# Kernel optimization log

Hardware: AMD Instinct MI355X
Metric: run time of the kernel (lower is better)

Reference implementation:

```python
import jax, jax.numpy as jnp
import numpy as np

N = 8192      # atoms
E = 4096      # edges (become transformer tokens)
E2 = 65536    # edges of second graph y
VOCAB = 119
DE = 200      # node_features == embedding_dim
D = 256
H = 8
L = 2
DFF = 2048


def _bn(x, g, b, eps=1e-6):
    m = x.mean(0)
    v = x.var(0)
    return (x - m) * jax.lax.rsqrt(v + eps) * g + b


def _ln(x, g, b, eps=1e-5):
    m = x.mean(-1, keepdims=True)
    v = ((x - m) ** 2).mean(-1, keepdims=True)
    return (x - m) * jax.lax.rsqrt(v + eps) * g + b


def _gcn(x, ei, W, b):
    # PyG GCNConv: add self loops, symmetric deg^-1/2 normalization
    n = x.shape[0]
    loop = jnp.arange(n)
    src = jnp.concatenate([ei[0], loop])
    dst = jnp.concatenate([ei[1], loop])
    deg = jax.ops.segment_sum(jnp.ones(src.shape[0], x.dtype), dst, num_segments=n)
    dinv = jnp.where(deg > 0, jax.lax.rsqrt(jnp.maximum(deg, 1e-12)), 0.0)
    msg = (x @ W)[src] * (dinv[src] * dinv[dst])[:, None]
    return jax.ops.segment_sum(msg, dst, num_segments=n) + b


def _mha(x, wi, bi, wo, bo):
    S, d = x.shape
    dh = d // H
    q, k, v = jnp.split(x @ wi + bi, 3, axis=1)
    q = q.reshape(S, H, dh)
    k = k.reshape(S, H, dh)
    v = v.reshape(S, H, dh)
    sc = jnp.einsum('qhd,khd->hqk', q, k) * (1.0 / np.sqrt(dh))
    a = jax.nn.softmax(sc, axis=-1)
    o = jnp.einsum('hqk,khd->qhd', a, v).reshape(S, d)
    return o @ wo + bo


def setup_inputs() -> dict:
    key = jax.random.key(0)
    ks = iter(jax.random.split(key, 64))
    nrm = lambda shape, s=0.05: jax.random.normal(next(ks), shape, jnp.float32) * s
    d = {}
    d['x'] = jax.random.randint(next(ks), (N,), 0, VOCAB)
    d['edge_index'] = jax.random.randint(next(ks), (2, E), 1, N + 1)  # 1-based, code subtracts 1
    d['pos'] = jax.random.normal(next(ks), (N, 3), jnp.float32)
    d['y'] = jax.random.randint(next(ks), (2, E2), 0, E)
    d['emb'] = nrm((VOCAB, DE), 1.0)
    d['fc1_w'] = nrm((1, DE))
    d['fc1_b'] = jnp.zeros((DE,), jnp.float32)
    d['bn4_g'] = jnp.ones((DE,), jnp.float32)
    d['bn4_b'] = jnp.zeros((DE,), jnp.float32)
    d['conv1_w'] = nrm((DE, D))
    d['conv1_b'] = jnp.zeros((D,), jnp.float32)
    d['conv2_w'] = nrm((D, D))
    d['conv2_b'] = jnp.zeros((D,), jnp.float32)
    for i in (1, 2, 3):
        d['bn%d_g' % i] = jnp.ones((D,), jnp.float32)
        d['bn%d_b' % i] = jnp.zeros((D,), jnp.float32)
    d['in_proj_w'] = nrm((L, D, 3 * D))
    d['in_proj_b'] = jnp.zeros((L, 3 * D), jnp.float32)
    d['out_proj_w'] = nrm((L, D, D))
    d['out_proj_b'] = jnp.zeros((L, D), jnp.float32)
    d['ln1_g'] = jnp.ones((L, D), jnp.float32)
    d['ln1_b'] = jnp.zeros((L, D), jnp.float32)
    d['ln2_g'] = jnp.ones((L, D), jnp.float32)
    d['ln2_b'] = jnp.zeros((L, D), jnp.float32)
    d['ff1_w'] = nrm((L, D, DFF))
    d['ff1_b'] = jnp.zeros((L, DFF), jnp.float32)
    d['ff2_w'] = nrm((L, DFF, D))
    d['ff2_b'] = jnp.zeros((L, D), jnp.float32)
    d['fc3_w'] = nrm((D, 1))
    d['fc3_b'] = jnp.zeros((1,), jnp.float32)
    d['fc4_w'] = nrm((D, 9))
    d['fc4_b'] = jnp.zeros((9,), jnp.float32)
    return d


def reference(x, edge_index, pos, y, emb, fc1_w, fc1_b, bn4_g, bn4_b,
              conv1_w, conv1_b, conv2_w, conv2_b,
              bn1_g, bn1_b, bn2_g, bn2_b, bn3_g, bn3_b,
              in_proj_w, in_proj_b, out_proj_w, out_proj_b,
              ln1_g, ln1_b, ln2_g, ln2_b, ff1_w, ff1_b, ff2_w, ff2_b,
              fc3_w, fc3_b, fc4_w, fc4_b):
    h = emb[x]                                   # [N, DE]
    ei = edge_index - 1
    row, col = ei[0], ei[1]
    ef = jnp.linalg.norm(pos[col] - pos[row], axis=1, keepdims=True)  # [E,1]
    ef = _bn(ef @ fc1_w + fc1_b, bn4_g, bn4_b)   # [E, DE]
    h = h[row] + h[col] + ef                     # [E, DE] edges -> tokens
    h = jax.nn.leaky_relu(_gcn(h, y, conv1_w, conv1_b))
    h = _bn(h, bn1_g, bn1_b)
    h = jax.nn.leaky_relu(h + _gcn(h, y, conv2_w, conv2_b))
    h = _bn(h, bn2_g, bn2_b)
    # post-norm TransformerEncoder (unbatched seq of length E), dropout=0
    for i in range(L):
        h = _ln(h + _mha(h, in_proj_w[i], in_proj_b[i], out_proj_w[i], out_proj_b[i]),
                ln1_g[i], ln1_b[i])
        ff = jax.nn.relu(h @ ff1_w[i] + ff1_b[i]) @ ff2_w[i] + ff2_b[i]
        h = _ln(h + ff, ln2_g[i], ln2_b[i])
    h = jax.nn.leaky_relu(h)
    h = _bn(h, bn3_g, bn3_b)
    sym_out = h @ fc3_w + fc3_b
    asym_out = h @ fc4_w + fc4_b
    return (sym_out, asym_out)
```

## Files before the change

### kernel.cpp

```cpp
#include <hip/hip_runtime.h>
#include <math.h>

#define ETOK 4096
#define NE2  65536
#define DEF  200
#define DM   256
#define NH   8
#define DH   32
#define DFFN 2048
#define NKS  8

#define QSCALE_LOG2E 0.25503474f

typedef __attribute__((ext_vector_type(8))) short bfrag8;
typedef __attribute__((ext_vector_type(4))) float f32x4;
typedef __attribute__((ext_vector_type(4))) short short4v;
typedef __attribute__((ext_vector_type(4))) unsigned int u32x4;

__device__ __forceinline__ unsigned short f2bf(float f) {
  union { float f; unsigned u; } v; v.f = f;
  unsigned u = v.u + 0x7fffu + ((v.u >> 16) & 1u);
  return (unsigned short)(u >> 16);
}
__device__ __forceinline__ float bf2f(unsigned short u) {
  union { unsigned u; float f; } v;
  v.u = ((unsigned)u) << 16;
  return v.f;
}
__device__ __forceinline__ unsigned cvt_pk_bf16(float lo, float hi) {
  unsigned r;
  asm("v_cvt_pk_bf16_f32 %0, %1, %2" : "=v"(r) : "v"(lo), "v"(hi));
  return r;
}

__device__ __forceinline__ float wave_sum(float v) {
#pragma unroll
  for (int off = 32; off > 0; off >>= 1) v += __shfl_xor(v, off);
  return v;
}
__device__ __forceinline__ float block_sum(float v, float* red) {
  v = wave_sum(v);
  int lane = threadIdx.x & 63, w = threadIdx.x >> 6;
  if (lane == 0) red[w] = v;
  __syncthreads();
  float t = red[0] + red[1] + red[2] + red[3];
  __syncthreads();
  return t;
}

__global__ void edge_deg_kernel(const int* __restrict__ ei, const float* __restrict__ pos,
                                float* __restrict__ ef0, float* __restrict__ stats,
                                const int* __restrict__ y, int* __restrict__ deg) {
  __shared__ float red[4];
  int e2 = blockIdx.x * 256 + threadIdx.x;
  atomicAdd(&deg[y[NE2 + e2]], 1);
  if (blockIdx.x < 16) {
    int e = blockIdx.x * 256 + threadIdx.x;
    int r = ei[e] - 1;
    int c = ei[ETOK + e] - 1;
    float dx = pos[c * 3 + 0] - pos[r * 3 + 0];
    float dy = pos[c * 3 + 1] - pos[r * 3 + 1];
    float dz = pos[c * 3 + 2] - pos[r * 3 + 2];
    float d = sqrtf(dx * dx + dy * dy + dz * dz);
    ef0[e] = d;
    float s = block_sum(d, red);
    float s2 = block_sum(d * d, red);
    if (threadIdx.x == 0) {
      atomicAdd(stats + 0, s);
      atomicAdd(stats + 1, s2);
    }
  }
}

__global__ void token_build_kernel(const int* __restrict__ x, const int* __restrict__ ei,
                                   const float* __restrict__ emb, const float* __restrict__ fc1_w,
                                   const float* __restrict__ bn4_g, const float* __restrict__ bn4_b,
                                   const float* __restrict__ ef0, const float* __restrict__ stats,
                                   unsigned short* __restrict__ tokbf) {
  int e = blockIdx.x;
  int j = threadIdx.x;
  float m = stats[0] * (1.0f / 4096.0f);
  float v = stats[1] * (1.0f / 4096.0f) - m * m;
  int xr = x[ei[e] - 1];
  int xc = x[ei[ETOK + e] - 1];
  float dd = ef0[e] - m;
  float val = 0.f;
  if (j < DEF) {
    float w = fc1_w[j];
    float s = w * rsqrtf(v * w * w + 1e-6f) * bn4_g[j];
    val = emb[(size_t)xr * DEF + j] + emb[(size_t)xc * DEF + j] + dd * s + bn4_b[j];
  }
  tokbf[(size_t)e * 256 + j] = f2bf(val);
}

__global__ void scan_kernel(const int* __restrict__ deg, int* __restrict__ off,
                            int* __restrict__ cursor, float* __restrict__ dinv) {
  __shared__ int part[256];
  int t = threadIdx.x;
  int v[16];
  int s = 0;
#pragma unroll
  for (int i = 0; i < 16; ++i) {
    v[i] = deg[t * 16 + i];
    s += v[i];
  }
  part[t] = s;
  __syncthreads();
  if (t == 0) {
    int a = 0;
#pragma unroll 1
    for (int i = 0; i < 256; ++i) {
      int tmp = part[i];
      part[i] = a;
      a += tmp;
    }
    off[4096] = a;
  }
  __syncthreads();
  int a = part[t];
#pragma unroll
  for (int i = 0; i < 16; ++i) {
    off[t * 16 + i] = a;
    cursor[t * 16 + i] = a;
    dinv[t * 16 + i] = rsqrtf((float)(v[i] + 1));
    a += v[i];
  }
}
__global__ void fill_kernel(const int* __restrict__ y, int* __restrict__ cursor,
                            int* __restrict__ srcl) {
  int e = blockIdx.x * 256 + threadIdx.x;
  int s = y[e];
  int d = y[NE2 + e];
  int slot = atomicAdd(&cursor[d], 1);
  srcl[slot] = s;
}

template <int RES, int ACT>
__global__ __launch_bounds__(256) void gather_kernel(const float* __restrict__ xw,
                                                     const int* __restrict__ off,
                                                     const int* __restrict__ srcl,
                                                     const float* __restrict__ dinv,
                                                     const float* __restrict__ bias,
                                                     const float* __restrict__ resid,
                                                     float* __restrict__ out) {
  __shared__ int slds[256];
  __shared__ float dlds[256];
  const int d = blockIdx.x;
  const int c = threadIdx.x;
  const int b0 = off[d], b1 = off[d + 1];
  const float dd = dinv[d];
  float acc = 0.f;
  for (int base = b0; base < b1; base += 256) {
    int n = min(256, b1 - base);
    __syncthreads();
    if (c < n) {
      int s = srcl[base + c];
      slds[c] = s;
      dlds[c] = dinv[s];
    }
    __syncthreads();
    for (int j = 0; j < n; ++j) {
      int s = slds[j];
      acc = fmaf(xw[(size_t)s * DM + c], dlds[j], acc);
    }
  }
  size_t idx = (size_t)d * DM + c;
  float v = bias[c] + xw[idx] * dd * dd + acc * dd;
  if (RES) v += resid[idx];
  if (ACT) v = v > 0.f ? v : 0.01f * v;
  out[idx] = v;
}

struct WEntry {
  const float* src;
  unsigned short* dst;
  int K, N, KP, tilesN, ntiles;
};
struct WPack {
  WEntry e[10];
};
__global__ __launch_bounds__(256) void wtrans_all_kernel(WPack p) {
  __shared__ float tl[32][33];
  int t = blockIdx.x;
  int i = 0;
  while (t >= p.e[i].ntiles) {
    t -= p.e[i].ntiles;
    ++i;
  }
  const WEntry w = p.e[i];
  int nb = (t % w.tilesN) * 32;
  int kb = (t / w.tilesN) * 32;
  int tx = threadIdx.x & 31, ty = threadIdx.x >> 5;
#pragma unroll
  for (int r = ty; r < 32; r += 8) {
    int k = kb + r, n = nb + tx;
    tl[r][tx] = (k < w.K && n < w.N) ? w.src[(size_t)k * w.N + n] : 0.f;
  }
  __syncthreads();
#pragma unroll
  for (int r = ty; r < 32; r += 8) {
    int n = nb + r, k = kb + tx;
    if (n < w.N) w.dst[(size_t)n * w.KP + k] = f2bf(tl[tx][r]);
  }
}

template <int BM, int BN, int OUTBF, int ACT, int QS, int VSPLIT>
__global__ __launch_bounds__(256) void mfma_gemm(const unsigned short* __restrict__ A,
                                                 const unsigned short* __restrict__ Bt,
                                                 const float* __restrict__ bias,
                                                 void* __restrict__ Cout, void* __restrict__ Cout2,
                                                 int M, int N, int K) {
  constexpr int BK = 64;
  constexpr int TM = BM / 32, TN = BN / 32;
  constexpr int ACH = BM / 32, BCH = BN / 32;
  __shared__ unsigned short Alds[BM * BK];
  __shared__ unsigned short Blds[BN * BK];
  const int tid = threadIdx.x;
  const int lane = tid & 63, wid = tid >> 6;
  const int g = lane >> 4, q = lane & 15;
  const int wr = wid >> 1, wc = wid & 1;
  const int m0 = blockIdx.y * BM, n0 = blockIdx.x * BN;

  f32x4 acc[TM][TN];
#pragma unroll
  for (int i = 0; i < TM; ++i)
#pragma unroll
    for (int j = 0; j < TN; ++j) acc[i][j] = (f32x4){0.f, 0.f, 0.f, 0.f};

  for (int k0 = 0; k0 < K; k0 += BK) {
    __syncthreads();
#pragma unroll
    for (int c = 0; c < ACH; ++c) {
      int chunk = wid * ACH + c;
      int row = chunk * 8 + (lane >> 3);
      int cb = ((lane & 7) * 16) ^ ((row & 7) << 4);
      const char* gp = (const char*)A + ((size_t)(m0 + row) * K + k0) * 2 + cb;
      __builtin_amdgcn_global_load_lds(
          (const __attribute__((address_space(1))) unsigned int*)gp,
          (__attribute__((address_space(3))) unsigned int*)(Alds + chunk * 512), 16, 0, 0);
    }
#pragma unroll
    for (int c = 0; c < BCH; ++c) {
      int chunk = wid * BCH + c;
      int row = chunk * 8 + (lane >> 3);
      int cb = ((lane & 7) * 16) ^ ((row & 7) << 4);
      const char* gp = (const char*)Bt + ((size_t)(n0 + row) * K + k0) * 2 + cb;
      __builtin_amdgcn_global_load_lds(
          (const __attribute__((address_space(1))) unsigned int*)gp,
          (__attribute__((address_space(3))) unsigned int*)(Blds + chunk * 512), 16, 0, 0);
    }
    __syncthreads();
#pragma unroll
    for (int ks = 0; ks < 2; ++ks) {
      bfrag8 af[TM], bfr[TN];
#pragma unroll
      for (int mi = 0; mi < TM; ++mi) {
        int row = wr * (BM / 2) + mi * 16 + q;
        int cb = (ks * 64 + g * 16) ^ ((row & 7) << 4);
        af[mi] = *(const bfrag8*)((const char*)Alds + row * 128 + cb);
      }
#pragma unroll
      for (int ni = 0; ni < TN; ++ni) {
        int row = wc * (BN / 2) + ni * 16 + q;
        int cb = (ks * 64 + g * 16) ^ ((row & 7) << 4);
        bfr[ni] = *(const bfrag8*)((const char*)Blds + row * 128 + cb);
      }
#pragma unroll
      for (int mi = 0; mi < TM; ++mi)
#pragma unroll
        for (int ni = 0; ni < TN; ++ni)
          acc[mi][ni] = __builtin_amdgcn_mfma_f32_16x16x32_bf16(af[mi], bfr[ni], acc[mi][ni], 0, 0, 0);
    }
  }
#pragma unroll
  for (int mi = 0; mi < TM; ++mi) {
    int row = m0 + wr * (BM / 2) + mi * 16 + g * 4;
#pragma unroll
    for (int ni = 0; ni < TN; ++ni) {
      int col = n0 + wc * (BN / 2) + ni * 16 + q;
      float bv = bias ? bias[col] : 0.f;
      if (VSPLIT && col >= 512) {
        short4v pkv;
#pragma unroll
        for (int r = 0; r < 4; ++r) pkv[r] = (short)f2bf(acc[mi][ni][r] + bv);
        *(short4v*)((unsigned short*)Cout2 + (size_t)(col - 512) * M + row) = pkv;
      } else {
#pragma unroll
        for (int r = 0; r < 4; ++r) {
          float v = acc[mi][ni][r] + bv;
          if (QS && col < DM) v *= QSCALE_LOG2E;
          if (ACT == 1) v = fmaxf(v, 0.f);
          if (OUTBF)
            ((unsigned short*)Cout)[(size_t)(row + r) * (VSPLIT ? 512 : N) + col] = f2bf(v);
          else
            ((float*)Cout)[(size_t)(row + r) * N + col] = v;
        }
      }
    }
  }
}

template <int LEAKY>
__global__ __launch_bounds__(256) void col_accum_kernel(const float* __restrict__ x,
                                                        float* __restrict__ colm,
                                                        float* __restrict__ colv) {
  int c = threadIdx.x;
  int r0 = blockIdx.x * 16;
  float s = 0.f, s2 = 0.f;
#pragma unroll
  for (int i = 0; i < 16; ++i) {
    float v = x[(size_t)(r0 + i) * DM + c];
    if (LEAKY) v = v > 0.f ? v : 0.01f * v;
    s += v;
    s2 += v * v;
  }
  atomicAdd(&colm[c], s);
  atomicAdd(&colv[c], s2);
}
template <int LEAKY>
__global__ void bn_apply_kernel(const float* __restrict__ x, const float* __restrict__ colm,
                                const float* __restrict__ colv, const float* __restrict__ g,
                                const float* __restrict__ b, float* __restrict__ outf,
                                unsigned short* __restrict__ outb, int C) {
  size_t i = (size_t)blockIdx.x * 256 + threadIdx.x;
  int c = (int)(i % C);
  float mean = colm[c] * (1.0f / 4096.0f);
  float var = colv[c] * (1.0f / 4096.0f) - mean * mean;
  float v0 = x[i];
  if (LEAKY) v0 = v0 > 0.f ? v0 : 0.01f * v0;
  float v = (v0 - mean) * rsqrtf(var + 1e-6f) * g[c] + b[c];
  outf[i] = v;
  if (outb) outb[i] = f2bf(v);
}

__global__ __launch_bounds__(256, 6) void attn_mfma_kernel(const unsigned short* __restrict__ qk,
                                                           const unsigned short* __restrict__ vt,
                                                           unsigned short* __restrict__ Opart,
                                                           float* __restrict__ Lpart) {
  const int h = blockIdx.y;
  const int qblk = blockIdx.x * 128;
  const int chunk = blockIdx.z;
  const int tid = threadIdx.x;
  const int wid = tid >> 6, lane = tid & 63;
  const int g = lane >> 4, q = lane & 15;

  __shared__ unsigned short Klds[64][40];
  __shared__ unsigned int Vtw[32][36];
  __shared__ unsigned short Plds[4][32][40];

  bfrag8 qfrag0, qfrag1;
  {
    const unsigned short* qp = qk + (size_t)(qblk + wid * 32 + q) * 512 + h * DH + g * 8;
    qfrag0 = *(const bfrag8*)qp;
    qfrag1 = *(const bfrag8*)(qp + 16 * 512);
  }
  bfrag8 ones;
#pragma unroll
  for (int i = 0; i < 8; ++i) ones[i] = (short)0x3F80;
  const f32x4 zero = {0.f, 0.f, 0.f, 0.f};

  const int skey = tid >> 2;
  const int sdb = (tid & 3) * 8;
  const int sd = tid >> 3;
  const int sk4 = (tid & 7) * 4;

  const int kbeg = chunk * (ETOK / NKS);
  const int NT = (ETOK / NKS) / 64;

  const unsigned short* kptr = qk + (size_t)(kbeg + skey) * 512 + DM + h * DH + sdb;
  const unsigned short* vptr = vt + (size_t)(h * DH + sd) * ETOK + kbeg + sk4 * 2;

  bfrag8 kreg = *(const bfrag8*)kptr;
  kptr += (size_t)64 * 512;
  u32x4 vreg = *(const u32x4*)vptr;
  vptr += 64;

  f32x4 o00 = zero, o01 = zero, o10 = zero, o11 = zero;
  f32x4 ol0 = zero, ol1 = zero;

  for (int t = 0; t < NT; ++t) {
    *(bfrag8*)&Klds[skey][sdb] = kreg;
    *(u32x4*)&Vtw[sd][sk4] = vreg;
    __syncthreads();
    if (t + 1 < NT) {
      kreg = *(const bfrag8*)kptr;
      kptr += (size_t)64 * 512;
      vreg = *(const u32x4*)vptr;
      vptr += 64;
    }

#pragma unroll
    for (int kg = 0; kg < 2; ++kg) {
      f32x4 s0a, s0b, s1a, s1b;
      __builtin_amdgcn_s_setprio(1);
      {
        bfrag8 kfa = *(const bfrag8*)&Klds[(2 * kg) * 16 + q][g * 8];
        bfrag8 kfb = *(const bfrag8*)&Klds[(2 * kg + 1) * 16 + q][g * 8];
        s0a = __builtin_amdgcn_mfma_f32_16x16x32_bf16(kfa, qfrag0, zero, 0, 0, 0);
        s1a = __builtin_amdgcn_mfma_f32_16x16x32_bf16(kfa, qfrag1, zero, 0, 0, 0);
        s0b = __builtin_amdgcn_mfma_f32_16x16x32_bf16(kfb, qfrag0, zero, 0, 0, 0);
        s1b = __builtin_amdgcn_mfma_f32_16x16x32_bf16(kfb, qfrag1, zero, 0, 0, 0);
      }
      __builtin_amdgcn_s_setprio(0);

      {
        uint2 w2;
        w2.x = cvt_pk_bf16(__builtin_exp2f(s0a[0]), __builtin_exp2f(s0a[1]));
        w2.y = cvt_pk_bf16(__builtin_exp2f(s0a[2]), __builtin_exp2f(s0a[3]));
        *(uint2*)&Plds[wid][q][g * 4] = w2;
        w2.x = cvt_pk_bf16(__builtin_exp2f(s0b[0]), __builtin_exp2f(s0b[1]));
        w2.y = cvt_pk_bf16(__builtin_exp2f(s0b[2]), __builtin_exp2f(s0b[3]));
        *(uint2*)&Plds[wid][q][16 + g * 4] = w2;
        w2.x = cvt_pk_bf16(__builtin_exp2f(s1a[0]), __builtin_exp2f(s1a[1]));
        w2.y = cvt_pk_bf16(__builtin_exp2f(s1a[2]), __builtin_exp2f(s1a[3]));
        *(uint2*)&Plds[wid][16 + q][g * 4] = w2;
        w2.x = cvt_pk_bf16(__builtin_exp2f(s1b[0]), __builtin_exp2f(s1b[1]));
        w2.y = cvt_pk_bf16(__builtin_exp2f(s1b[2]), __builtin_exp2f(s1b[3]));
        *(uint2*)&Plds[wid][16 + q][16 + g * 4] = w2;
      }

      __builtin_amdgcn_s_setprio(1);
      {
        bfrag8 pa0 = *(const bfrag8*)&Plds[wid][q][g * 8];
        bfrag8 pa1 = *(const bfrag8*)&Plds[wid][16 + q][g * 8];
        bfrag8 vb0 = *(const bfrag8*)&Vtw[q][kg * 16 + g * 4];
        bfrag8 vb1 = *(const bfrag8*)&Vtw[16 + q][kg * 16 + g * 4];
        o00 = __builtin_amdgcn_mfma_f32_16x16x32_bf16(pa0, vb0, o00, 0, 0, 0);
        o01 = __builtin_amdgcn_mfma_f32_16x16x32_bf16(pa0, vb1, o01, 0, 0, 0);
        o10 = __builtin_amdgcn_mfma_f32_16x16x32_bf16(pa1, vb0, o10, 0, 0, 0);
        o11 = __builtin_amdgcn_mfma_f32_16x16x32_bf16(pa1, vb1, o11, 0, 0, 0);
        ol0 = __builtin_amdgcn_mfma_f32_16x16x32_bf16(pa0, ones, ol0, 0, 0, 0);
        ol1 = __builtin_amdgcn_mfma_f32_16x16x32_bf16(pa1, ones, ol1, 0, 0, 0);
      }
      __builtin_amdgcn_s_setprio(0);
    }
    __syncthreads();
  }

#pragma unroll
  for (int r = 0; r < 4; ++r) {
    int row0 = qblk + wid * 32 + g * 4 + r;
    unsigned short* op0 = Opart + ((size_t)chunk * ETOK + row0) * DM + h * DH;
    op0[q] = f2bf(o00[r]);
    op0[16 + q] = f2bf(o01[r]);
    unsigned short* op1 = op0 + (size_t)16 * DM;
    op1[q] = f2bf(o10[r]);
    op1[16 + q] = f2bf(o11[r]);
  }
  if (q == 0) {
#pragma unroll
    for (int r = 0; r < 4; ++r) {
      int row = qblk + wid * 32 + g * 4 + r;
      Lpart[((size_t)chunk * ETOK + row) * NH + h] = ol0[r];
      Lpart[((size_t)chunk * ETOK + row + 16) * NH + h] = ol1[r];
    }
  }
}

__global__ __launch_bounds__(256) void attn_combine_kernel(const unsigned short* __restrict__ Opart,
                                                           const float* __restrict__ Lpart,
                                                           unsigned short* __restrict__ out) {
  __shared__ float ls[NKS][NH];
  const int row = blockIdx.x;
  const int c = threadIdx.x;
  if (c < NKS * NH) {
    ls[c >> 3][c & 7] = Lpart[((size_t)(c >> 3) * ETOK + row) * NH + (c & 7)];
  }
  __syncthreads();
  const int h = c >> 5;
  float lstar = 0.f, acc = 0.f;
#pragma unroll
  for (int ch = 0; ch < NKS; ++ch) {
    lstar += ls[ch][h];
    acc += bf2f(Opart[((size_t)ch * ETOK + row) * DM + c]);
  }
  out[(size_t)row * DM + c] = f2bf(acc / lstar);
}

__global__ void add_ln_kernel(const float* __restrict__ x, const float* __restrict__ r,
                              float* __restrict__ outf, unsigned short* __restrict__ outb,
                              const float* __restrict__ g, const float* __restrict__ b) {
  __shared__ float red[4];
  int row = blockIdx.x, t = threadIdx.x;
  size_t idx = (size_t)row * DM + t;
  float v = x[idx] + r[idx];
  float mean = block_sum(v, red) * (1.0f / 256.0f);
  float dv = v - mean;
  float var = block_sum(dv * dv, red) * (1.0f / 256.0f);
  float o = dv * rsqrtf(var + 1e-5f) * g[t] + b[t];
  outf[idx] = o;
  outb[idx] = f2bf(o);
}

__global__ void head_kernel(const float* __restrict__ h, const float* __restrict__ colm,
                            const float* __restrict__ colv, const float* __restrict__ bng,
                            const float* __restrict__ bnb, const float* __restrict__ fc3w,
                            const float* __restrict__ fc3b, const float* __restrict__ fc4w,
                            const float* __restrict__ fc4b, float* __restrict__ out) {
  int wave = threadIdx.x >> 6, lane = threadIdx.x & 63;
  int tok = blockIdx.x * 4 + wave;
  const float* hr = h + (size_t)tok * DM;
  float hv[4];
#pragma unroll
  for (int i = 0; i < 4; ++i) {
    int col = lane * 4 + i;
    float v = hr[col];
    v = v > 0.f ? v : 0.01f * v;
    float mean = colm[col] * (1.0f / 4096.0f);
    float var = colv[col] * (1.0f / 4096.0f) - mean * mean;
    hv[i] = (v - mean) * rsqrtf(var + 1e-6f) * bng[col] + bnb[col];
  }
  float acc = 0.f;
#pragma unroll
  for (int i = 0; i < 4; ++i) acc += hv[i] * fc3w[lane * 4 + i];
  acc = wave_sum(acc);
  if (lane == 0) out[tok] = acc + fc3b[0];
#pragma unroll
  for (int j = 0; j < 9; ++j) {
    float a = 0.f;
#pragma unroll
    for (int i = 0; i < 4; ++i) a += hv[i] * fc4w[(lane * 4 + i) * 9 + j];
    a = wave_sum(a);
    if (lane == 0) out[ETOK + (size_t)tok * 9 + j] = a + fc4b[j];
  }
}

extern "C" void kernel_launch(void* const* d_in, const int* in_sizes, int n_in,
                              void* d_out, int out_size, void* d_ws, size_t ws_size,
                              hipStream_t stream) {
  const int* x = (const int*)d_in[0];
  const int* edge_index = (const int*)d_in[1];
  const float* pos = (const float*)d_in[2];
  const int* y = (const int*)d_in[3];
  const float* emb = (const float*)d_in[4];
  const float* fc1_w = (const float*)d_in[5];
  const float* bn4_g = (const float*)d_in[7];
  const float* bn4_b = (const float*)d_in[8];
  const float* conv1_w = (const float*)d_in[9];
  const float* conv1_b = (const float*)d_in[10];
  const float* conv2_w = (const float*)d_in[11];
  const float* conv2_b = (const float*)d_in[12];
  const float* bn1_g = (const float*)d_in[13];
  const float* bn1_b = (const float*)d_in[14];
  const float* bn2_g = (const float*)d_in[15];
  const float* bn2_b = (const float*)d_in[16];
  const float* bn3_g = (const float*)d_in[17];
  const float* bn3_b = (const float*)d_in[18];
  const float* ipw = (const float*)d_in[19];
  const float* ipb = (const float*)d_in[20];
  const float* opw = (const float*)d_in[21];
  const float* opb = (const float*)d_in[22];
  const float* ln1_g = (const float*)d_in[23];
  const float* ln1_b = (const float*)d_in[24];
  const float* ln2_g = (const float*)d_in[25];
  const float* ln2_b = (const float*)d_in[26];
  const float* ff1w = (const float*)d_in[27];
  const float* ff1b = (const float*)d_in[28];
  const float* ff2w = (const float*)d_in[29];
  const float* ff2b = (const float*)d_in[30];
  const float* fc3w = (const float*)d_in[31];
  const float* fc3b = (const float*)d_in[32];
  const float* fc4w = (const float*)d_in[33];
  const float* fc4b = (const float*)d_in[34];
  float* outp = (float*)d_out;

  char* wsp = (char*)d_ws;
  auto alloc = [&](size_t bytes) {
    void* p = (void*)wsp;
    wsp += (bytes + 255) & ~(size_t)255;
    return p;
  };
  unsigned short* big_bf = (unsigned short*)alloc((size_t)ETOK * DFFN * 2);
  unsigned short* qk_bf = (unsigned short*)alloc((size_t)ETOK * 512 * 2);
  unsigned short* vt_bf = (unsigned short*)alloc((size_t)DM * ETOK * 2);
  unsigned short* attno = (unsigned short*)alloc((size_t)ETOK * DM * 2);
  unsigned short* h_bf = (unsigned short*)alloc((size_t)ETOK * DM * 2);
  unsigned short* tok_bf = (unsigned short*)alloc((size_t)ETOK * 256 * 2);
  float* hf = (float*)alloc((size_t)ETOK * DM * 4);
  float* t1 = (float*)alloc((size_t)ETOK * DM * 4);
  float* t2 = (float*)alloc((size_t)ETOK * DM * 4);
  unsigned short* Opart = (unsigned short*)alloc((size_t)NKS * ETOK * DM * 2);
  float* Lpart = (float*)alloc((size_t)NKS * ETOK * NH * 4);
  unsigned short* c1wt = (unsigned short*)alloc(256 * 256 * 2);
  unsigned short* c2wt = (unsigned short*)alloc(256 * 256 * 2);
  unsigned short* ipwt = (unsigned short*)alloc((size_t)2 * 768 * 256 * 2);
  unsigned short* opwt = (unsigned short*)alloc((size_t)2 * 256 * 256 * 2);
  unsigned short* f1wt = (unsigned short*)alloc((size_t)2 * 2048 * 256 * 2);
  unsigned short* f2wt = (unsigned short*)alloc((size_t)2 * 256 * 2048 * 2);
  float* ef0 = (float*)alloc(ETOK * 4);
  float* dinv = (float*)alloc(ETOK * 4);
  int* off = (int*)alloc((ETOK + 1) * 4);
  int* cursor = (int*)alloc(ETOK * 4);
  int* srcl = (int*)alloc(NE2 * 4);
  char* z0 = wsp;
  float* stats = (float*)alloc(8 * 4);
  float* colm = (float*)alloc(3 * DM * 4);
  float* colv = (float*)alloc(3 * DM * 4);
  int* deg = (int*)alloc(ETOK * 4);
  size_t zlen = (char*)wsp - z0;

  hipMemsetAsync(z0, 0, zlen, stream);

  WPack wp;
  int ntot = 0;
  auto went = [&](int i, const float* src, unsigned short* dst, int K, int N, int KP) {
    wp.e[i].src = src;
    wp.e[i].dst = dst;
    wp.e[i].K = K;
    wp.e[i].N = N;
    wp.e[i].KP = KP;
    wp.e[i].tilesN = (N + 31) / 32;
    wp.e[i].ntiles = ((N + 31) / 32) * (KP / 32);
    ntot += wp.e[i].ntiles;
  };
  went(0, conv1_w, c1wt, 200, 256, 256);
  went(1, conv2_w, c2wt, 256, 256, 256);
  went(2, ipw, ipwt, 256, 768, 256);
  went(3, ipw + (size_t)256 * 768, ipwt + (size_t)768 * 256, 256, 768, 256);
  went(4, opw, opwt, 256, 256, 256);
  went(5, opw + (size_t)256 * 256, opwt + (size_t)256 * 256, 256, 256, 256);
  went(6, ff1w, f1wt, 256, 2048, 256);
  went(7, ff1w + (size_t)256 * 2048, f1wt + (size_t)2048 * 256, 256, 2048, 256);
  went(8, ff2w, f2wt, 2048, 256, 2048);
  went(9, ff2w + (size_t)2048 * 256, f2wt + (size_t)256 * 2048, 2048, 256, 2048);
  wtrans_all_kernel<<<ntot, 256, 0, stream>>>(wp);

  edge_deg_kernel<<<NE2 / 256, 256, 0, stream>>>(edge_index, pos, ef0, stats, y, deg);
  scan_kernel<<<1, 256, 0, stream>>>(deg, off, cursor, dinv);
  fill_kernel<<<NE2 / 256, 256, 0, stream>>>(y, cursor, srcl);
  token_build_kernel<<<ETOK, 256, 0, stream>>>(x, edge_index, emb, fc1_w, bn4_g, bn4_b, ef0,
                                               stats, tok_bf);

  mfma_gemm<64, 32, 0, 0, 0, 0><<<dim3(8, 64), 256, 0, stream>>>(tok_bf, c1wt, nullptr, t1,
                                                                 nullptr, ETOK, DM, 256);
  gather_kernel<0, 1><<<ETOK, 256, 0, stream>>>(t1, off, srcl, dinv, conv1_b, nullptr, t2);
  col_accum_kernel<0><<<ETOK / 16, 256, 0, stream>>>(t2, colm, colv);
  bn_apply_kernel<0><<<ETOK * DM / 256, 256, 0, stream>>>(t2, colm, colv, bn1_g, bn1_b, hf, h_bf, DM);

  mfma_gemm<64, 32, 0, 0, 0, 0><<<dim3(8, 64), 256, 0, stream>>>(h_bf, c2wt, nullptr, t1,
                                                                 nullptr, ETOK, DM, 256);
  gather_kernel<1, 1><<<ETOK, 256, 0, stream>>>(t1, off, srcl, dinv, conv2_b, hf, t2);
  col_accum_kernel<0><<<ETOK / 16, 256, 0, stream>>>(t2, colm + DM, colv + DM);
  bn_apply_kernel<0><<<ETOK * DM / 256, 256, 0, stream>>>(t2, colm + DM, colv + DM, bn2_g, bn2_b,
                                                          hf, h_bf, DM);

  for (int i = 0; i < 2; ++i) {
    mfma_gemm<64, 32, 1, 0, 1, 1><<<dim3(24, 64), 256, 0, stream>>>(
        h_bf, ipwt + (size_t)i * 768 * 256, ipb + (size_t)i * 768, qk_bf, vt_bf, ETOK, 768, 256);
    attn_mfma_kernel<<<dim3(ETOK / 128, NH, NKS), 256, 0, stream>>>(qk_bf, vt_bf, Opart, Lpart);
    attn_combine_kernel<<<ETOK, 256, 0, stream>>>(Opart, Lpart, attno);
    mfma_gemm<64, 32, 0, 0, 0, 0><<<dim3(8, 64), 256, 0, stream>>>(
        attno, opwt + (size_t)i * 256 * 256, opb + (size_t)i * DM, t2, nullptr, ETOK, DM, 256);
    add_ln_kernel<<<ETOK, 256, 0, stream>>>(t2, hf, hf, h_bf, ln1_g + (size_t)i * DM,
                                            ln1_b + (size_t)i * DM);
    mfma_gemm<64, 64, 1, 1, 0, 0><<<dim3(32, 64), 256, 0, stream>>>(
        h_bf, f1wt + (size_t)i * 2048 * 256, ff1b + (size_t)i * DFFN, big_bf, nullptr, ETOK, DFFN, 256);
    mfma_gemm<64, 32, 0, 0, 0, 0><<<dim3(8, 64), 256, 0, stream>>>(
        big_bf, f2wt + (size_t)i * 256 * 2048, ff2b + (size_t)i * DM, t2, nullptr, ETOK, DM, 2048);
    add_ln_kernel<<<ETOK, 256, 0, stream>>>(t2, hf, hf, h_bf, ln2_g + (size_t)i * DM,
                                            ln2_b + (size_t)i * DM);
  }

  col_accum_kernel<1><<<ETOK / 16, 256, 0, stream>>>(hf, colm + 2 * DM, colv + 2 * DM);
  head_kernel<<<ETOK / 4, 256, 0, stream>>>(hf, colm + 2 * DM, colv + 2 * DM, bn3_g, bn3_b,
                                            fc3w, fc3b, fc4w, fc4b, outp);
}
```

Measured before the change: 321.4 us.

## Double attention query tile per block to reuse K/V tiles across more queries

```diff
diff --git a/kernel.cpp b/kernel.cpp
--- a/kernel.cpp
+++ b/kernel.cpp
@@ -333,12 +333,12 @@
   if (outb) outb[i] = f2bf(v);
 }
 
-__global__ __launch_bounds__(256, 6) void attn_mfma_kernel(const unsigned short* __restrict__ qk,
+__global__ __launch_bounds__(256, 4) void attn_mfma_kernel(const unsigned short* __restrict__ qk,
                                                            const unsigned short* __restrict__ vt,
                                                            unsigned short* __restrict__ Opart,
                                                            float* __restrict__ Lpart) {
   const int h = blockIdx.y;
-  const int qblk = blockIdx.x * 128;
+  const int qblk = blockIdx.x * 256;
   const int chunk = blockIdx.z;
   const int tid = threadIdx.x;
   const int wid = tid >> 6, lane = tid & 63;
@@ -346,13 +346,14 @@
 
   __shared__ unsigned short Klds[64][40];
   __shared__ unsigned int Vtw[32][36];
-  __shared__ unsigned short Plds[4][32][40];
-
-  bfrag8 qfrag0, qfrag1;
-  {
-    const unsigned short* qp = qk + (size_t)(qblk + wid * 32 + q) * 512 + h * DH + g * 8;
-    qfrag0 = *(const bfrag8*)qp;
-    qfrag1 = *(const bfrag8*)(qp + 16 * 512);
+  __shared__ unsigned short Plds[4][16][40];
+
+  bfrag8 qfrag[4];
+#pragma unroll
+  for (int qf = 0; qf < 4; ++qf) {
+    const unsigned short* qp =
+        qk + (size_t)(qblk + wid * 64 + qf * 16 + q) * 512 + h * DH + g * 8;
+    qfrag[qf] = *(const bfrag8*)qp;
   }
   bfrag8 ones;
 #pragma unroll
@@ -375,8 +376,14 @@
   u32x4 vreg = *(const u32x4*)vptr;
   vptr += 64;
 
-  f32x4 o00 = zero, o01 = zero, o10 = zero, o11 = zero;
-  f32x4 ol0 = zero, ol1 = zero;
+  f32x4 o[4][2];
+  f32x4 ol[4];
+#pragma unroll
+  for (int qf = 0; qf < 4; ++qf) {
+    o[qf][0] = zero;
+    o[qf][1] = zero;
+    ol[qf] = zero;
+  }
 
   for (int t = 0; t < NT; ++t) {
     *(bfrag8*)&Klds[skey][sdb] = kreg;
@@ -390,69 +397,57 @@
     }
 
 #pragma unroll
-    for (int kg = 0; kg < 2; ++kg) {
-      f32x4 s0a, s0b, s1a, s1b;
+    for (int qf = 0; qf < 4; ++qf) {
+      f32x4 s[4];
       __builtin_amdgcn_s_setprio(1);
-      {
-        bfrag8 kfa = *(const bfrag8*)&Klds[(2 * kg) * 16 + q][g * 8];
-        bfrag8 kfb = *(const bfrag8*)&Klds[(2 * kg + 1) * 16 + q][g * 8];
-        s0a = __builtin_amdgcn_mfma_f32_16x16x32_bf16(kfa, qfrag0, zero, 0, 0, 0);
-        s1a = __builtin_amdgcn_mfma_f32_16x16x32_bf16(kfa, qfrag1, zero, 0, 0, 0);
-        s0b = __builtin_amdgcn_mfma_f32_16x16x32_bf16(kfb, qfrag0, zero, 0, 0, 0);
-        s1b = __builtin_amdgcn_mfma_f32_16x16x32_bf16(kfb, qfrag1, zero, 0, 0, 0);
+#pragma unroll
+      for (int tt = 0; tt < 4; ++tt) {
+        bfrag8 kf = *(const bfrag8*)&Klds[tt * 16 + q][g * 8];
+        s[tt] = __builtin_amdgcn_mfma_f32_16x16x32_bf16(kf, qfrag[qf], zero, 0, 0, 0);
       }
       __builtin_amdgcn_s_setprio(0);
 
-      {
-        uint2 w2;
-        w2.x = cvt_pk_bf16(__builtin_exp2f(s0a[0]), __builtin_exp2f(s0a[1]));
-        w2.y = cvt_pk_bf16(__builtin_exp2f(s0a[2]), __builtin_exp2f(s0a[3]));
-        *(uint2*)&Plds[wid][q][g * 4] = w2;
-        w2.x = cvt_pk_bf16(__builtin_exp2f(s0b[0]), __builtin_exp2f(s0b[1]));
-        w2.y = cvt_pk_bf16(__builtin_exp2f(s0b[2]), __builtin_exp2f(s0b[3]));
-        *(uint2*)&Plds[wid][q][16 + g * 4] = w2;
-        w2.x = cvt_pk_bf16(__builtin_exp2f(s1a[0]), __builtin_exp2f(s1a[1]));
-        w2.y = cvt_pk_bf16(__builtin_exp2f(s1a[2]), __builtin_exp2f(s1a[3]));
-        *(uint2*)&Plds[wid][16 + q][g * 4] = w2;
-        w2.x = cvt_pk_bf16(__builtin_exp2f(s1b[0]), __builtin_exp2f(s1b[1]));
-        w2.y = cvt_pk_bf16(__builtin_exp2f(s1b[2]), __builtin_exp2f(s1b[3]));
-        *(uint2*)&Plds[wid][16 + q][16 + g * 4] = w2;
+#pragma unroll
+      for (int kg = 0; kg < 2; ++kg) {
+        {
+          uint2 w2;
+          w2.x = cvt_pk_bf16(__builtin_exp2f(s[2 * kg][0]), __builtin_exp2f(s[2 * kg][1]));
+          w2.y = cvt_pk_bf16(__builtin_exp2f(s[2 * kg][2]), __builtin_exp2f(s[2 * kg][3]));
+          *(uint2*)&Plds[wid][q][g * 4] = w2;
+          w2.x = cvt_pk_bf16(__builtin_exp2f(s[2 * kg + 1][0]), __builtin_exp2f(s[2 * kg + 1][1]));
+          w2.y = cvt_pk_bf16(__builtin_exp2f(s[2 * kg + 1][2]), __builtin_exp2f(s[2 * kg + 1][3]));
+          *(uint2*)&Plds[wid][q][16 + g * 4] = w2;
+        }
+        __builtin_amdgcn_s_setprio(1);
+        {
+          bfrag8 pa = *(const bfrag8*)&Plds[wid][q][g * 8];
+          bfrag8 vb0 = *(const bfrag8*)&Vtw[q][kg * 16 + g * 4];
+          bfrag8 vb1 = *(const bfrag8*)&Vtw[16 + q][kg * 16 + g * 4];
+          o[qf][0] = __builtin_amdgcn_mfma_f32_16x16x32_bf16(pa, vb0, o[qf][0], 0, 0, 0);
+          o[qf][1] = __builtin_amdgcn_mfma_f32_16x16x32_bf16(pa, vb1, o[qf][1], 0, 0, 0);
+          ol[qf] = __builtin_amdgcn_mfma_f32_16x16x32_bf16(pa, ones, ol[qf], 0, 0, 0);
+        }
+        __builtin_amdgcn_s_setprio(0);
       }
-
-      __builtin_amdgcn_s_setprio(1);
-      {
-        bfrag8 pa0 = *(const bfrag8*)&Plds[wid][q][g * 8];
-        bfrag8 pa1 = *(const bfrag8*)&Plds[wid][16 + q][g * 8];
-        bfrag8 vb0 = *(const bfrag8*)&Vtw[q][kg * 16 + g * 4];
-        bfrag8 vb1 = *(const bfrag8*)&Vtw[16 + q][kg * 16 + g * 4];
-        o00 = __builtin_amdgcn_mfma_f32_16x16x32_bf16(pa0, vb0, o00, 0, 0, 0);
-        o01 = __builtin_amdgcn_mfma_f32_16x16x32_bf16(pa0, vb1, o01, 0, 0, 0);
-        o10 = __builtin_amdgcn_mfma_f32_16x16x32_bf16(pa1, vb0, o10, 0, 0, 0);
-        o11 = __builtin_amdgcn_mfma_f32_16x16x32_bf16(pa1, vb1, o11, 0, 0, 0);
-        ol0 = __builtin_amdgcn_mfma_f32_16x16x32_bf16(pa0, ones, ol0, 0, 0, 0);
-        ol1 = __builtin_amdgcn_mfma_f32_16x16x32_bf16(pa1, ones, ol1, 0, 0, 0);
+    }
+    __syncthreads();
+  }
+
+#pragma unroll
+  for (int qf = 0; qf < 4; ++qf) {
+#pragma unroll
+    for (int r = 0; r < 4; ++r) {
+      int row0 = qblk + wid * 64 + qf * 16 + g * 4 + r;
+      unsigned short* op = Opart + ((size_t)chunk * ETOK + row0) * DM + h * DH;
+      op[q] = f2bf(o[qf][0][r]);
+      op[16 + q] = f2bf(o[qf][1][r]);
+    }
+    if (q == 0) {
+#pragma unroll
+      for (int r = 0; r < 4; ++r) {
+        int row = qblk + wid * 64 + qf * 16 + g * 4 + r;
+        Lpart[((size_t)chunk * ETOK + row) * NH + h] = ol[qf][r];
       }
-      __builtin_amdgcn_s_setprio(0);
-    }
-    __syncthreads();
-  }
-
-#pragma unroll
-  for (int r = 0; r < 4; ++r) {
-    int row0 = qblk + wid * 32 + g * 4 + r;
-    unsigned short* op0 = Opart + ((size_t)chunk * ETOK + row0) * DM + h * DH;
-    op0[q] = f2bf(o00[r]);
-    op0[16 + q] = f2bf(o01[r]);
-    unsigned short* op1 = op0 + (size_t)16 * DM;
-    op1[q] = f2bf(o10[r]);
-    op1[16 + q] = f2bf(o11[r]);
-  }
-  if (q == 0) {
-#pragma unroll
-    for (int r = 0; r < 4; ++r) {
-      int row = qblk + wid * 32 + g * 4 + r;
-      Lpart[((size_t)chunk * ETOK + row) * NH + h] = ol0[r];
-      Lpart[((size_t)chunk * ETOK + row + 16) * NH + h] = ol1[r];
     }
   }
 }
@@ -647,7 +642,7 @@
   for (int i = 0; i < 2; ++i) {
     mfma_gemm<64, 32, 1, 0, 1, 1><<<dim3(24, 64), 256, 0, stream>>>(
         h_bf, ipwt + (size_t)i * 768 * 256, ipb + (size_t)i * 768, qk_bf, vt_bf, ETOK, 768, 256);
-    attn_mfma_kernel<<<dim3(ETOK / 128, NH, NKS), 256, 0, stream>>>(qk_bf, vt_bf, Opart, Lpart);
+    attn_mfma_kernel<<<dim3(ETOK / 256, NH, NKS), 256, 0, stream>>>(qk_bf, vt_bf, Opart, Lpart);
     attn_combine_kernel<<<ETOK, 256, 0, stream>>>(Opart, Lpart, attno);
     mfma_gemm<64, 32, 0, 0, 0, 0><<<dim3(8, 64), 256, 0, stream>>>(
         attno, opwt + (size_t)i * 256 * 256, opb + (size_t)i * DM, t2, nullptr, ETOK, DM, 256);
```

After: 329.2 us. 1.02x slower.
